# Kernel tuning notes

Hardware: AMD Instinct MI355X
Metric: run time of the kernel (lower is better)

The kernel has to match this reference:

```python
import jax, jax.numpy as jnp
import numpy as np

DN = ('NCHW', 'OIHW', 'NCHW')
EPS = 1e-5


def _conv(x, w, b, stride, pad):
    y = jax.lax.conv_general_dilated(x, w, (stride, stride), ((pad, pad), (pad, pad)), dimension_numbers=DN)
    return y + b[None, :, None, None]


def _convT(x, w, b):
    # PyTorch ConvTranspose2d(k=3, stride=2, padding=1, output_padding=1)
    # weight w: [in, out, kh, kw] -> flip spatial, swap in/out -> OIHW
    wt = jnp.flip(w, (2, 3)).transpose(1, 0, 2, 3)
    y = jax.lax.conv_general_dilated(x, wt, (1, 1), ((1, 2), (1, 2)), lhs_dilation=(2, 2), dimension_numbers=DN)
    return y + b[None, :, None, None]


def _inorm(x):
    # InstanceNorm2d, affine=False, biased variance (num_features arg unused since no affine)
    m = x.mean((2, 3), keepdims=True)
    v = ((x - m) ** 2).mean((2, 3), keepdims=True)
    return (x - m) / jnp.sqrt(v + EPS)


def _lrelu(x):
    return jnp.where(x >= 0, x, 0.2 * x)


def _refpad(x):
    return jnp.pad(x, ((0, 0), (0, 0), (1, 1), (1, 1)), mode='reflect')


def _backbone(image, w1, b1, w2, b2, w3, b3, wt, bt, w4, b4):
    x = _lrelu(_inorm(_conv(_refpad(image), w1, b1, 1, 0)))   # [B,32,H,W]
    x = _lrelu(_inorm(_conv(x, w2, b2, 2, 1)))                 # [B,64,H/2,W/2]
    x = _lrelu(_inorm(_conv(x, w3, b3, 2, 1)))                 # [B,128,H/4,W/4]
    x = _lrelu(_inorm(_convT(x, wt, bt)))                      # [B,256,H/2,W/2]
    x = jnp.tanh(_conv(_refpad(x), w4, b4, 1, 0))              # [B,512,H/2,W/2]
    return x


def _style_codes(x, seg):
    # nearest interpolation of seg to (h,w): src_idx = floor(dst * H / h)
    B, C, h, w = x.shape
    H, W = seg.shape[2], seg.shape[3]
    rows = (np.arange(h) * H) // h
    cols = (np.arange(w) * W) // w
    seg_ds = seg[:, :, rows][:, :, :, cols]                    # [B,L,h,w]
    m = (seg_ds != 0).astype(x.dtype)
    sums = jnp.einsum('bchw,blhw->blc', x, m)                  # segment sums
    counts = m.sum((2, 3))[..., None]                          # [B,L,1]
    return jnp.where(counts > 0, sums / jnp.maximum(counts, 1.0), 0.0)


def setup_inputs():
    key = jax.random.key(0)
    ks = jax.random.split(key, 8)
    B, H, W, L = 8, 256, 256, 19
    image = jax.random.normal(ks[0], (B, 3, H, W), jnp.float32)
    labels = jax.random.randint(ks[1], (B, H, W), 0, L)
    seg = jax.nn.one_hot(labels, L, axis=1, dtype=jnp.float32)  # one-hot semantic map
    def w(k, shape):
        return jax.random.normal(k, shape, jnp.float32) * 0.05
    return {
        'image': image, 'seg': seg,
        'w1': w(ks[2], (32, 3, 3, 3)), 'b1': jnp.zeros(32, jnp.float32),
        'w2': w(ks[3], (64, 32, 3, 3)), 'b2': jnp.zeros(64, jnp.float32),
        'w3': w(ks[4], (128, 64, 3, 3)), 'b3': jnp.zeros(128, jnp.float32),
        'wt': w(ks[5], (128, 256, 3, 3)), 'bt': jnp.zeros(256, jnp.float32),
        'w4': w(ks[6], (512, 256, 3, 3)), 'b4': jnp.zeros(512, jnp.float32),
    }


def reference(image, seg, w1, b1, w2, b2, w3, b3, wt, bt, w4, b4):
    x = _backbone(image, w1, b1, w2, b2, w3, b3, wt, bt, w4, b4)
    return _style_codes(x, seg)  # [B, label_nc, 512]
```

## Files before the change

### kernel.cpp

```cpp
#include <hip/hip_runtime.h>
#include <hip/hip_bf16.h>
#include <math.h>

typedef __attribute__((ext_vector_type(8))) short bf16x8;
typedef __attribute__((ext_vector_type(8))) unsigned short u16x8;
typedef __attribute__((ext_vector_type(4))) float f32x4;
typedef __attribute__((ext_vector_type(2))) long longx2;

#define OFF_X1   0ull
#define OFF_XQ8  0ull
#define OFF_X2   34080768ull
#define OFF_X3   51386368ull
#define OFF_Y4   60039168ull
#define OFF_WB8  127148032ull
#define OFF_WB2  129507328ull
#define OFF_WB3  129548288ull
#define OFF_WBT  129695744ull
#define OFF_ST1  130744320ull
#define OFF_ST2  130746368ull
#define OFF_ST3  130750464ull
#define OFF_ST4  130758656ull
#define OFF_SUMS 130775040ull
#define OFF_CNT  131086336ull
#define OFF_MS1  131086944ull
#define OFF_MS2  131088992ull
#define OFF_MS3  131093088ull
#define OFF_MS4  131101280ull
#define OFF_LAB  131117664ull
#define OFF_DWS  131641952ull
#define OFF_WSM  132166240ull
#define OFF_ST5  132690528ull
#define OFF_CB   132706912ull

__device__ __forceinline__ float bfu2f(unsigned short u) {
  return __builtin_bit_cast(float, ((unsigned)u) << 16);
}
__device__ __forceinline__ unsigned short f2bfu(float f) {
  __hip_bfloat16 h = __float2bfloat16(f);
  return __builtin_bit_cast(unsigned short, h);
}
__device__ __forceinline__ void gload_lds16(const void* g, void* l) {
  __builtin_amdgcn_global_load_lds(
      (const __attribute__((address_space(1))) unsigned int*)g,
      (__attribute__((address_space(3))) unsigned int*)l, 16, 0, 0);
}
template <bool HI>
__device__ __forceinline__ int cvtpk8(float a, float b, int old) {
  return __builtin_amdgcn_cvt_pk_fp8_f32(a, b, old, HI);
}
template <int SEL>
__device__ __forceinline__ float cvtf8(int v) {
  return __builtin_amdgcn_cvt_f32_fp8(v, SEL);
}

#define WAITV(N) asm volatile("s_waitcnt vmcnt(" #N ")" ::: "memory")

#define PIPE_STEP(WAITN, BUF, DOSTAGE, SNEXT)                 \
  asm volatile("s_waitcnt vmcnt(" #WAITN ")" ::: "memory");   \
  __builtin_amdgcn_s_barrier();                               \
  __builtin_amdgcn_sched_barrier(0);                          \
  mmaStep(BUF, (BUF) + 16384);                                \
  __builtin_amdgcn_sched_barrier(0);                          \
  __builtin_amdgcn_s_barrier();                               \
  if (DOSTAGE) stage(SNEXT, BUF);

__global__ __launch_bounds__(256) void conv1_k(const float* __restrict__ img,
                                               const float* __restrict__ w1,
                                               unsigned short* __restrict__ x1) {
  __shared__ float wl[864];
  int t = threadIdx.x, y = blockIdx.x, b = blockIdx.y;
  for (int i = t; i < 864; i += 256) wl[i] = w1[(i & 31) * 27 + (i >> 5)];
  __syncthreads();
  int x = t;
  float val[27];
  for (int ic = 0; ic < 3; ++ic) {
    const float* ip = img + ((size_t)(b * 3 + ic)) * 65536;
#pragma unroll
    for (int ky = 0; ky < 3; ++ky) {
      int gy = y - 1 + ky; gy = gy < 0 ? -gy : (gy > 255 ? 510 - gy : gy);
#pragma unroll
      for (int kx = 0; kx < 3; ++kx) {
        int gx = x - 1 + kx; gx = gx < 0 ? -gx : (gx > 255 ? 510 - gx : gx);
        val[ic * 9 + ky * 3 + kx] = ip[gy * 256 + gx];
      }
    }
  }
  float a[32];
#pragma unroll
  for (int oc = 0; oc < 32; ++oc) a[oc] = 0.f;
#pragma unroll
  for (int k = 0; k < 27; ++k) {
    float vv = val[k];
#pragma unroll
    for (int oc = 0; oc < 32; ++oc) a[oc] += wl[k * 32 + oc] * vv;
  }
  unsigned short ov[32];
#pragma unroll
  for (int oc = 0; oc < 32; ++oc) ov[oc] = f2bfu(a[oc]);
  unsigned short* op = x1 + ((size_t)(b * 258 + y + 1) * 258 + (x + 1)) * 32;
#pragma unroll
  for (int i = 0; i < 4; ++i) *(u16x8*)(op + i * 8) = *(const u16x8*)(ov + i * 8);
}

template <int C>
__global__ void statsn_k(const unsigned short* __restrict__ base, int rowStride, int unitsLog,
                         int rowsPer, long bStride, float* __restrict__ stats) {
  const int CH8 = C / 8;
  __shared__ float bins[C * 2];
  int tid = threadIdx.x, slice = blockIdx.x, b = blockIdx.y;
  for (int i = tid; i < C * 2; i += 256) bins[i] = 0.f;
  __syncthreads();
  const unsigned short* bp = base + (size_t)b * bStride + (size_t)(slice * rowsPer) * rowStride;
  int total = rowsPer << unitsLog;
  float s8[8] = {0, 0, 0, 0, 0, 0, 0, 0}, q8[8] = {0, 0, 0, 0, 0, 0, 0, 0};
  for (int idx = tid; idx < total; idx += 256) {
    int rl = idx >> unitsLog, ux = idx & ((1 << unitsLog) - 1);
    u16x8 v = *(const u16x8*)(bp + (size_t)rl * rowStride + ux * 8);
#pragma unroll
    for (int e = 0; e < 8; ++e) { float f = bfu2f(v[e]); s8[e] += f; q8[e] += f * f; }
  }
#pragma unroll
  for (int e = 0; e < 8; ++e)
    for (int off = 32; off >= CH8; off >>= 1) {
      s8[e] += __shfl_xor(s8[e], off);
      q8[e] += __shfl_xor(q8[e], off);
    }
  int lane = tid & 63;
  if (lane < CH8) {
#pragma unroll
    for (int e = 0; e < 8; ++e) {
      atomicAdd(&bins[(lane * 8 + e) * 2], s8[e]);
      atomicAdd(&bins[(lane * 8 + e) * 2 + 1], q8[e]);
    }
  }
  __syncthreads();
  for (int i = tid; i < C * 2; i += 256) atomicAdd(&stats[b * C * 2 + i], bins[i]);
}

__global__ void msn_k(const float* __restrict__ st, float2* __restrict__ ms, float invN, int total) {
  int i = blockIdx.x * 256 + threadIdx.x;
  if (i < total) {
    float m = st[2 * i] * invN;
    float v = st[2 * i + 1] * invN - m * m;
    ms[i] = make_float2(m, rsqrtf(fmaxf(v, 0.f) + 1e-5f));
  }
}

template <int C>
__global__ void nln_k(unsigned short* __restrict__ base, int rowStride, int unitsPerRow,
                      long bStride, const float2* __restrict__ ms) {
  const int CH8 = C / 8;
  int row = blockIdx.x, b = blockIdx.y;
  unsigned short* rp = base + (size_t)b * bStride + (size_t)row * rowStride;
  const float2* msb = ms + b * C;
  for (int idx = threadIdx.x; idx < unitsPerRow; idx += 256) {
    u16x8 v = *(u16x8*)(rp + idx * 8);
    int ch = (idx & (CH8 - 1)) * 8;
    u16x8 o;
#pragma unroll
    for (int e = 0; e < 8; ++e) {
      float2 m = msb[ch + e];
      float f = (bfu2f(v[e]) - m.x) * m.y;
      o[e] = f2bfu(f >= 0.f ? f : 0.2f * f);
    }
    *(u16x8*)(rp + idx * 8) = o;
  }
}

__global__ __launch_bounds__(256) void nln8_k(const unsigned short* __restrict__ y4,
                                              const float2* __restrict__ ms,
                                              unsigned char* __restrict__ xq8,
                                              float* __restrict__ st5) {
  __shared__ float bs[512];
  int t = threadIdx.x, row = blockIdx.x, b = blockIdx.y;
  int cg = t & 31, pg = t >> 5;
  int wof0 = (cg >> 4) * 128 + ((((cg & 15) & 3) << 2) | ((cg & 15) >> 2)) * 8;
  const float2* msb = ms + b * 256;
  float2 m0[8];
#pragma unroll
  for (int e = 0; e < 8; ++e) m0[e] = msb[cg * 8 + e];
  const unsigned short* rp = y4 + ((size_t)b * 16384 + row * 128) * 256;
  unsigned char* op = xq8 + ((size_t)b * 16384 + (size_t)row * 128) * 256;
  float s[8] = {0, 0, 0, 0, 0, 0, 0, 0}, d[8] = {0, 0, 0, 0, 0, 0, 0, 0};
  for (int i = 0; i < 16; ++i) {
    int px = pg * 16 + i;
    u16x8 v = *(const u16x8*)(rp + (size_t)px * 256 + cg * 8);
    float f[8];
#pragma unroll
    for (int e = 0; e < 8; ++e) {
      float x = (bfu2f(v[e]) - m0[e].x) * m0[e].y;
      f[e] = x >= 0.f ? x : 0.2f * x;
    }
    int lo = cvtpk8<false>(f[0], f[1], 0); lo = cvtpk8<true>(f[2], f[3], lo);
    int hi = cvtpk8<false>(f[4], f[5], 0); hi = cvtpk8<true>(f[6], f[7], hi);
    *(int*)(op + (size_t)px * 256 + wof0) = lo;
    *(int*)(op + (size_t)px * 256 + wof0 + 4) = hi;
    float fq;
    fq = cvtf8<0>(lo); s[0] += fq; d[0] += fq - f[0];
    fq = cvtf8<1>(lo); s[1] += fq; d[1] += fq - f[1];
    fq = cvtf8<2>(lo); s[2] += fq; d[2] += fq - f[2];
    fq = cvtf8<3>(lo); s[3] += fq; d[3] += fq - f[3];
    fq = cvtf8<0>(hi); s[4] += fq; d[4] += fq - f[4];
    fq = cvtf8<1>(hi); s[5] += fq; d[5] += fq - f[5];
    fq = cvtf8<2>(hi); s[6] += fq; d[6] += fq - f[6];
    fq = cvtf8<3>(hi); s[7] += fq; d[7] += fq - f[7];
  }
  for (int i = t; i < 512; i += 256) bs[i] = 0.f;
  __syncthreads();
#pragma unroll
  for (int e = 0; e < 8; ++e) {
    atomicAdd(&bs[cg * 8 + e], s[e]);
    atomicAdd(&bs[256 + cg * 8 + e], d[e]);
  }
  __syncthreads();
  for (int i = t; i < 512; i += 256) atomicAdd(&st5[b * 512 + i], bs[i]);
}

__global__ void wrep2_k(const float* __restrict__ w2, unsigned short* __restrict__ wb2) {
  int idx = blockIdx.x * 256 + threadIdx.x;
  if (idx >= 20480) return;
  int oc = idx / 320, r = idx % 320, tap = r >> 5, ic = r & 31;
  wb2[idx] = tap < 9 ? f2bfu(w2[(oc * 32 + ic) * 9 + tap]) : (unsigned short)0;
}
__global__ void wrep3_k(const float* __restrict__ w3, unsigned short* __restrict__ wb3) {
  int idx = blockIdx.x * 256 + threadIdx.x;
  int oc = idx / 576, r = idx % 576, tap = r >> 6, ic = r & 63;
  wb3[idx] = f2bfu(w3[(oc * 64 + ic) * 9 + tap]);
}
__device__ const int c_taptab[16] = {4, -1, -1, -1, 5, 3, -1, -1, 7, -1, 1, -1, 8, 6, 2, 0};
__global__ void wrepT_k(const float* __restrict__ wt, unsigned short* __restrict__ wbt) {
  int idx = blockIdx.x * 256 + threadIdx.x;
  int n = idx >> 9, k = idx & 511;
  int cl = n >> 8, oc = n & 255, nb = k >> 7, ic = k & 127;
  int tap = c_taptab[cl * 4 + nb];
  wbt[idx] = tap < 0 ? (unsigned short)0 : f2bfu(wt[(ic * 256 + oc) * 9 + tap]);
}
__global__ __launch_bounds__(256) void dwrep_k(const float* __restrict__ w4,
                                               unsigned char* __restrict__ wb8,
                                               float* __restrict__ dws,
                                               float* __restrict__ wsum) {
  int oc = blockIdx.x, ic = threadIdx.x;
  int local = ic & 127;
  int p = (ic & 128) + ((local >> 3) & 3) * 32 + ((local >> 5) & 3) * 8 + (local & 7);
  float ds = 0.f, ws = 0.f;
  for (int kk = 0; kk < 9; ++kk) {
    float w = w4[(size_t)oc * 2304 + ic * 9 + kk];
    int pk = cvtpk8<false>(w, 0.f, 0);
    wb8[((size_t)oc * 9 + kk) * 256 + p] = (unsigned char)(pk & 0xff);
    float wq = cvtf8<0>(pk);
    ds += wq - w; ws += w;
  }
  dws[oc * 256 + ic] = ds;
  wsum[oc * 256 + ic] = ws;
}

__global__ __launch_bounds__(256) void cbias_k(const float* __restrict__ st5,
                                               const float* __restrict__ dws,
                                               const float* __restrict__ wsum,
                                               float* __restrict__ cb) {
  int oc = blockIdx.x, b = blockIdx.y, t = threadIdx.x;
  const float inv = 1.f / 16384.f;
  float muq = st5[b * 512 + t] * inv;
  float dmu = st5[b * 512 + 256 + t] * inv;
  float a = muq * dws[oc * 256 + t] + dmu * wsum[oc * 256 + t];
#pragma unroll
  for (int o = 1; o < 64; o <<= 1) a += __shfl_xor(a, o);
  __shared__ float r[4];
  if ((t & 63) == 0) r[t >> 6] = a;
  __syncthreads();
  if (t == 0) cb[b * 512 + oc] = r[0] + r[1] + r[2] + r[3];
}

__global__ __launch_bounds__(256) void conv2_k(const unsigned short* __restrict__ x1,
                                               const unsigned short* __restrict__ wb2,
                                               unsigned short* __restrict__ x2,
                                               float* __restrict__ st2) {
  __shared__ char smem[49664];
  float* bins = (float*)(smem + 49152);
  int tid = threadIdx.x, y = blockIdx.x, b = blockIdx.y;
  int lane = tid & 63, w = tid >> 6, wm = w >> 1, wn = w & 1;
  int lr = lane & 15, lg = lane >> 4;
  f32x4 acc[4][2];
#pragma unroll
  for (int i = 0; i < 4; ++i)
#pragma unroll
    for (int j = 0; j < 2; ++j) acc[i][j] = (f32x4){0.f, 0.f, 0.f, 0.f};

  int rowA[4], lcA[4], PbA[4];
#pragma unroll
  for (int i = 0; i < 4; ++i) {
    int pb = i * 256 + tid;
    PbA[i] = pb * 16; rowA[i] = pb >> 3; lcA[i] = (pb & 7) ^ (rowA[i] & 7);
  }
  int rowB[2], lcB[2], PbB[2];
#pragma unroll
  for (int i = 0; i < 2; ++i) {
    int pb = i * 256 + tid;
    PbB[i] = pb * 16; rowB[i] = pb >> 3; lcB[i] = (pb & 7) ^ (rowB[i] & 7);
  }
  const unsigned short* xb = x1 + (size_t)b * 2130048;

  auto stage = [&](int kb, char* base) {
    char* As = base;
    char* Bs = base + 16384;
#pragma unroll
    for (int i = 0; i < 4; ++i) {
      int tp = kb * 2 + (lcA[i] >> 2);
      int ky = (tp * 11) >> 5;
      int kx = tp - ky * 3;
      gload_lds16(xb + ((size_t)((2 * y + ky) * 258 + 2 * rowA[i] + kx)) * 32 + (lcA[i] & 3) * 8,
                  As + PbA[i]);
    }
#pragma unroll
    for (int i = 0; i < 2; ++i)
      gload_lds16(wb2 + rowB[i] * 320 + kb * 64 + lcB[i] * 8, Bs + PbB[i]);
  };

  stage(0, smem);
  __syncthreads();
  for (int kb = 0; kb < 5; ++kb) {
    char* base = smem + (kb & 1) * 24576;
    if (kb + 1 < 5) stage(kb + 1, smem + ((kb + 1) & 1) * 24576);
    char* As = base;
    char* Bs = base + 16384;
    bf16x8 af[4][2], bfr[2][2];
#pragma unroll
    for (int mi = 0; mi < 4; ++mi)
#pragma unroll
      for (int kh = 0; kh < 2; ++kh) {
        int row = wm * 64 + mi * 16 + lr;
        int byte = row * 128 + ((kh * 64 + lg * 16) ^ ((row & 7) << 4));
        af[mi][kh] = *(const bf16x8*)(As + byte);
      }
#pragma unroll
    for (int ni = 0; ni < 2; ++ni)
#pragma unroll
      for (int kh = 0; kh < 2; ++kh) {
        int row = wn * 32 + ni * 16 + lr;
        int byte = row * 128 + ((kh * 64 + lg * 16) ^ ((row & 7) << 4));
        bfr[ni][kh] = *(const bf16x8*)(Bs + byte);
      }
#pragma unroll
    for (int mi = 0; mi < 4; ++mi)
#pragma unroll
      for (int ni = 0; ni < 2; ++ni)
#pragma unroll
        for (int kh = 0; kh < 2; ++kh)
          acc[mi][ni] = __builtin_amdgcn_mfma_f32_16x16x32_bf16(af[mi][kh], bfr[ni][kh],
                                                                acc[mi][ni], 0, 0, 0);
    __syncthreads();
  }

  if (tid < 128) bins[tid] = 0.f;
  __syncthreads();
  unsigned short* ob = x2 + (size_t)b * 1081600;
#pragma unroll
  for (int ni = 0; ni < 2; ++ni) {
    int oc = wn * 32 + ni * 16 + lr;
    float s = 0.f, q = 0.f;
#pragma unroll
    for (int mi = 0; mi < 4; ++mi)
#pragma unroll
      for (int r = 0; r < 4; ++r) {
        int m = wm * 64 + mi * 16 + lg * 4 + r;
        float v = acc[mi][ni][r];
        ob[((y + 1) * 130 + m + 1) * 64 + oc] = f2bfu(v);
        s += v; q += v * v;
      }
    atomicAdd(&bins[oc * 2], s);
    atomicAdd(&bins[oc * 2 + 1], q);
  }
  __syncthreads();
  if (tid < 128) atomicAdd(&st2[b * 128 + tid], bins[tid]);
}

__global__ __launch_bounds__(256) void conv3_k(const unsigned short* __restrict__ x2,
                                               const unsigned short* __restrict__ wb3,
                                               unsigned short* __restrict__ x3,
                                               float* __restrict__ st3) {
  __shared__ char smem[66560];
  float* bins = (float*)(smem + 65536);
  int tid = threadIdx.x, y0 = blockIdx.x * 2, b = blockIdx.y;
  int lane = tid & 63, w = tid >> 6, wm = w >> 1, wn = w & 1;
  int lr = lane & 15, lg = lane >> 4;
  f32x4 acc[4][4];
#pragma unroll
  for (int i = 0; i < 4; ++i)
#pragma unroll
    for (int j = 0; j < 4; ++j) acc[i][j] = (f32x4){0.f, 0.f, 0.f, 0.f};

  int rowS[4], lc[4], Pb[4];
#pragma unroll
  for (int i = 0; i < 4; ++i) {
    int pb = i * 256 + tid;
    Pb[i] = pb * 16; rowS[i] = pb >> 3; lc[i] = (pb & 7) ^ (rowS[i] & 7);
  }
  const unsigned short* xb = x2 + (size_t)b * 1081600;

  auto stage = [&](int kk, char* base) {
    int ky = kk / 3, kx = kk - ky * 3;
#pragma unroll
    for (int i = 0; i < 4; ++i) {
      int m = rowS[i], di = m >> 6, xx = m & 63;
      gload_lds16(xb + ((size_t)((2 * (y0 + di) + ky) * 130 + 2 * xx + kx)) * 64 + lc[i] * 8,
                  base + Pb[i]);
    }
#pragma unroll
    for (int i = 0; i < 4; ++i)
      gload_lds16(wb3 + (rowS[i] * 9 + kk) * 64 + lc[i] * 8, base + 16384 + Pb[i]);
  };

  stage(0, smem);
  __syncthreads();
  for (int kk = 0; kk < 9; ++kk) {
    char* base = smem + (kk & 1) * 32768;
    if (kk + 1 < 9) stage(kk + 1, smem + ((kk + 1) & 1) * 32768);
    char* As = base;
    char* Bs = base + 16384;
    bf16x8 af[4][2], bfr[4][2];
#pragma unroll
    for (int mi = 0; mi < 4; ++mi)
#pragma unroll
      for (int kh = 0; kh < 2; ++kh) {
        int row = wm * 64 + mi * 16 + lr;
        int byte = row * 128 + ((kh * 64 + lg * 16) ^ ((row & 7) << 4));
        af[mi][kh] = *(const bf16x8*)(As + byte);
      }
#pragma unroll
    for (int ni = 0; ni < 4; ++ni)
#pragma unroll
      for (int kh = 0; kh < 2; ++kh) {
        int row = wn * 64 + ni * 16 + lr;
        int byte = row * 128 + ((kh * 64 + lg * 16) ^ ((row & 7) << 4));
        bfr[ni][kh] = *(const bf16x8*)(Bs + byte);
      }
#pragma unroll
    for (int mi = 0; mi < 4; ++mi)
#pragma unroll
      for (int ni = 0; ni < 4; ++ni)
#pragma unroll
        for (int kh = 0; kh < 2; ++kh)
          acc[mi][ni] = __builtin_amdgcn_mfma_f32_16x16x32_bf16(af[mi][kh], bfr[ni][kh],
                                                                acc[mi][ni], 0, 0, 0);
    __syncthreads();
  }

  if (tid < 256) bins[tid] = 0.f;
  __syncthreads();
  unsigned short* ob = x3 + (size_t)b * 540800;
#pragma unroll
  for (int ni = 0; ni < 4; ++ni) {
    int oc = wn * 64 + ni * 16 + lr;
    float s = 0.f, q = 0.f;
#pragma unroll
    for (int mi = 0; mi < 4; ++mi)
#pragma unroll
      for (int r = 0; r < 4; ++r) {
        int m = wm * 64 + mi * 16 + lg * 4 + r;
        int di = m >> 6, xx = m & 63;
        float v = acc[mi][ni][r];
        ob[((y0 + di) * 65 + xx) * 128 + oc] = f2bfu(v);
        s += v; q += v * v;
      }
    atomicAdd(&bins[oc * 2], s);
    atomicAdd(&bins[oc * 2 + 1], q);
  }
  __syncthreads();
  if (tid < 256) atomicAdd(&st3[b * 256 + tid], bins[tid]);
}

__global__ __launch_bounds__(256) void convT_k(const unsigned short* __restrict__ x3,
                                               const unsigned short* __restrict__ wbt,
                                               unsigned short* __restrict__ y4,
                                               float* __restrict__ st4) {
  __shared__ char smem[67584];
  float* bins = (float*)(smem + 65536);
  int tid = threadIdx.x, i0 = blockIdx.x * 2, nblk = blockIdx.y, b = blockIdx.z;
  int n0 = nblk * 128, cl = nblk >> 1, och0 = (nblk & 1) * 128;
  int lane = tid & 63, w = tid >> 6, wm = w >> 1, wn = w & 1;
  int lr = lane & 15, lg = lane >> 4;
  f32x4 acc[4][4];
#pragma unroll
  for (int i = 0; i < 4; ++i)
#pragma unroll
    for (int j = 0; j < 4; ++j) acc[i][j] = (f32x4){0.f, 0.f, 0.f, 0.f};

  int rowS[4], lc[4], Pb[4];
#pragma unroll
  for (int i = 0; i < 4; ++i) {
    int pb = i * 256 + tid;
    Pb[i] = pb * 16; rowS[i] = pb >> 3; lc[i] = (pb & 7) ^ (rowS[i] & 7);
  }
  int aoff[4][2], boff[4][2];
#pragma unroll
  for (int mi = 0; mi < 4; ++mi)
#pragma unroll
    for (int kh = 0; kh < 2; ++kh) {
      int row = wm * 64 + mi * 16 + lr;
      aoff[mi][kh] = row * 128 + ((kh * 64 + lg * 16) ^ ((row & 7) << 4));
      int rowb = wn * 64 + mi * 16 + lr;
      boff[mi][kh] = rowb * 128 + ((kh * 64 + lg * 16) ^ ((rowb & 7) << 4));
    }
  const unsigned short* xb = x3 + (size_t)b * 540800;

  auto stage = [&](int kb, char* base) {
    int nb = kb >> 1, chalf = (kb & 1) * 64;
#pragma unroll
    for (int i = 0; i < 4; ++i) {
      int m = rowS[i], di = m >> 6, j = m & 63;
      int pi = i0 + di + (nb >> 1), pj = j + (nb & 1);
      gload_lds16(xb + ((size_t)(pi * 65 + pj)) * 128 + chalf + lc[i] * 8, base + Pb[i]);
    }
#pragma unroll
    for (int i = 0; i < 4; ++i)
      gload_lds16(wbt + (size_t)(n0 + rowS[i]) * 512 + kb * 64 + lc[i] * 8,
                  base + 16384 + Pb[i]);
  };

  auto mmaStep = [&](char* As, char* Bs) {
    bf16x8 af[4][2], bfr[4][2];
#pragma unroll
    for (int mi = 0; mi < 4; ++mi)
#pragma unroll
      for (int kh = 0; kh < 2; ++kh) af[mi][kh] = *(const bf16x8*)(As + aoff[mi][kh]);
#pragma unroll
    for (int ni = 0; ni < 4; ++ni)
#pragma unroll
      for (int kh = 0; kh < 2; ++kh) bfr[ni][kh] = *(const bf16x8*)(Bs + boff[ni][kh]);
#pragma unroll
    for (int mi = 0; mi < 4; ++mi)
#pragma unroll
      for (int ni = 0; ni < 4; ++ni)
#pragma unroll
        for (int kh = 0; kh < 2; ++kh)
          acc[mi][ni] = __builtin_amdgcn_mfma_f32_16x16x32_bf16(af[mi][kh], bfr[ni][kh],
                                                                acc[mi][ni], 0, 0, 0);
  };

  char* B0 = smem;
  char* B1 = smem + 32768;
  stage(0, B0);
  stage(1, B1);
  for (int sp = 0; sp < 3; ++sp) {
    PIPE_STEP(8, B0, true, 2 * sp + 2);
    PIPE_STEP(8, B1, true, 2 * sp + 3);
  }
  PIPE_STEP(8, B0, false, 0);
  PIPE_STEP(0, B1, false, 0);

  if (tid < 256) bins[tid] = 0.f;
  __syncthreads();
  unsigned short* ob = y4 + (size_t)b * 4194304;
  int dy = cl >> 1, dx = cl & 1;
#pragma unroll
  for (int ni = 0; ni < 4; ++ni) {
    int loc = wn * 64 + ni * 16 + lr;
    int oc = och0 + loc;
    float s = 0.f, q = 0.f;
#pragma unroll
    for (int mi = 0; mi < 4; ++mi)
#pragma unroll
      for (int r = 0; r < 4; ++r) {
        int m = wm * 64 + mi * 16 + lg * 4 + r;
        int di = m >> 6, j = m & 63;
        int oy = 2 * (i0 + di) + dy, ox = 2 * j + dx;
        float v = acc[mi][ni][r];
        ob[(oy * 128 + ox) * 256 + oc] = f2bfu(v);
        s += v; q += v * v;
      }
    atomicAdd(&bins[loc * 2], s);
    atomicAdd(&bins[loc * 2 + 1], q);
  }
  __syncthreads();
  if (tid < 256) atomicAdd(&st4[b * 512 + och0 * 2 + tid], bins[tid]);
}

__global__ void lab_k(const float* __restrict__ seg, int* __restrict__ lab,
                      float* __restrict__ counts) {
  __shared__ int hist[19];
  int t = threadIdx.x;
  if (t < 19) hist[t] = 0;
  __syncthreads();
  int b = blockIdx.y;
  int p = blockIdx.x * 256 + t;
  int i = p >> 7, j = p & 127;
  const float* sp = seg + (size_t)b * 19 * 65536 + (2 * i) * 256 + 2 * j;
  int l = 0;
  for (int k = 0; k < 19; ++k) { if (sp[(size_t)k * 65536] != 0.f) { l = k; break; } }
  lab[b * 16384 + p] = l;
  atomicAdd(&hist[l], 1);
  __syncthreads();
  if (t < 19) atomicAdd(&counts[b * 19 + t], (float)hist[t]);
}

__global__ __launch_bounds__(256, 3) void conv4_k(
    const unsigned char* __restrict__ xq8, const unsigned char* __restrict__ wb8,
    const float* __restrict__ b4, const float* __restrict__ cb,
    const int* __restrict__ lab, float* __restrict__ sums) {
  __shared__ char smem[33280];
  char* As = smem;
  char* Bs = smem + 16384;
  int* labs = (int*)(smem + 32768);
  int tid = threadIdx.x;
  int id = blockIdx.x;
  int b = id & 7, rr = id >> 3;
  int y = rr >> 2, nblk = rr & 3;
  int n0 = nblk * 128;
  if (tid < 128) labs[tid] = lab[b * 16384 + y * 128 + tid];
  int lane = tid & 63, w = tid >> 6;
  int wm = w >> 1, wn = w & 1;
  int lr = lane & 15, lg = lane >> 4;

  f32x4 acc[4][4];
#pragma unroll
  for (int i = 0; i < 4; ++i)
#pragma unroll
    for (int j = 0; j < 4; ++j) acc[i][j] = (f32x4){0.f, 0.f, 0.f, 0.f};

  const unsigned char* xb = xq8 + (size_t)b * 4194304;

  int rs0 = tid >> 3;
  int csw = ((tid & 7) ^ (rs0 & 7)) << 4;
  int ldoff = tid * 16;

  const unsigned char* brow[4];
#pragma unroll
  for (int i = 0; i < 4; ++i)
    brow[i] = wb8 + (size_t)(n0 + rs0 + 32 * i) * 2304 + csw;

  int koff = 0;
  for (int kk = 0; kk < 9; ++kk) {
    int ky = (kk * 11) >> 5, kx = kk - ky * 3;
    int sy = y + ky - 1; sy = sy < 0 ? 1 : (sy > 127 ? 126 : sy);
    const unsigned char* arow[4];
#pragma unroll
    for (int i = 0; i < 4; ++i) {
      int sx = rs0 + 32 * i + kx - 1;
      sx = sx < 0 ? 1 : (sx > 127 ? 126 : sx);
      arow[i] = xb + ((size_t)(sy * 128 + sx)) * 256 + csw;
    }
    for (int ic0 = 0; ic0 < 256; ic0 += 128) {
      __syncthreads();
#pragma unroll
      for (int i = 0; i < 4; ++i) gload_lds16(arow[i] + ic0, As + i * 4096 + ldoff);
#pragma unroll
      for (int i = 0; i < 4; ++i) gload_lds16(brow[i] + koff, Bs + i * 4096 + ldoff);
      koff += 128;
      __syncthreads();

      longx2 bq[4][2];
#pragma unroll
      for (int ni = 0; ni < 4; ++ni) {
        int row = wn * 64 + ni * 16 + lr;
#pragma unroll
        for (int k2 = 0; k2 < 2; ++k2) {
          int byte = row * 128 + ((lg * 32 + k2 * 16) ^ ((row & 7) << 4));
          bq[ni][k2] = *(const longx2*)(Bs + byte);
        }
      }
#pragma unroll
      for (int mi = 0; mi < 4; ++mi) {
        int row = wm * 64 + mi * 16 + lr;
        longx2 aq[2];
#pragma unroll
        for (int k2 = 0; k2 < 2; ++k2) {
          int byte = row * 128 + ((lg * 32 + k2 * 16) ^ ((row & 7) << 4));
          aq[k2] = *(const longx2*)(As + byte);
        }
#pragma unroll
        for (int ni = 0; ni < 4; ++ni)
#pragma unroll
          for (int k2 = 0; k2 < 2; ++k2) {
            acc[mi][ni] = __builtin_amdgcn_mfma_f32_16x16x32_fp8_fp8(
                aq[k2][0], bq[ni][k2][0], acc[mi][ni], 0, 0, 0);
            acc[mi][ni] = __builtin_amdgcn_mfma_f32_16x16x32_fp8_fp8(
                aq[k2][1], bq[ni][k2][1], acc[mi][ni], 0, 0, 0);
          }
      }
    }
  }

  __syncthreads();
  float* bins = (float*)smem;
  for (int t2 = tid; t2 < 19 * 128; t2 += 256) bins[t2] = 0.f;
  __syncthreads();
  float bias[4];
#pragma unroll
  for (int ni = 0; ni < 4; ++ni) {
    int gc = n0 + wn * 64 + ni * 16 + lr;
    bias[ni] = b4[gc] - cb[b * 512 + gc];
  }
#pragma unroll
  for (int mi = 0; mi < 4; ++mi)
#pragma unroll
    for (int ni = 0; ni < 4; ++ni) {
      int ct = wn * 64 + ni * 16 + lr;
#pragma unroll
      for (int r = 0; r < 4; ++r) {
        int x = wm * 64 + mi * 16 + lg * 4 + r;
        float v = tanhf(acc[mi][ni][r] + bias[ni]);
        atomicAdd(&bins[labs[x] * 128 + ct], v);
      }
    }
  __syncthreads();
  for (int t2 = tid; t2 < 19 * 128; t2 += 256) {
    float v = bins[t2];
    if (v != 0.f)
      atomicAdd(&sums[((size_t)(b * 19 + (t2 >> 7))) * 512 + n0 + (t2 & 127)], v);
  }
}

__global__ void finalize_k(const float* __restrict__ sums, const float* __restrict__ counts,
                           float* __restrict__ out) {
  int idx = blockIdx.x * 256 + threadIdx.x;
  int bl = idx / 512;
  float c = counts[bl];
  out[idx] = c > 0.f ? sums[idx] / fmaxf(c, 1.f) : 0.f;
}

extern "C" void kernel_launch(void* const* d_in, const int* in_sizes, int n_in,
                              void* d_out, int out_size, void* d_ws, size_t ws_size,
                              hipStream_t stream) {
  const float* image = (const float*)d_in[0];
  const float* seg   = (const float*)d_in[1];
  const float* w1    = (const float*)d_in[2];
  const float* w2    = (const float*)d_in[4];
  const float* w3    = (const float*)d_in[6];
  const float* wt    = (const float*)d_in[8];
  const float* w4    = (const float*)d_in[10];
  const float* b4    = (const float*)d_in[11];
  float* out = (float*)d_out;
  char* ws = (char*)d_ws;

  unsigned short* x1  = (unsigned short*)(ws + OFF_X1);
  unsigned char*  xq8 = (unsigned char*)(ws + OFF_XQ8);
  unsigned short* x2  = (unsigned short*)(ws + OFF_X2);
  unsigned short* x3  = (unsigned short*)(ws + OFF_X3);
  unsigned short* y4  = (unsigned short*)(ws + OFF_Y4);
  unsigned char*  wb8 = (unsigned char*)(ws + OFF_WB8);
  unsigned short* wb2 = (unsigned short*)(ws + OFF_WB2);
  unsigned short* wb3 = (unsigned short*)(ws + OFF_WB3);
  unsigned short* wbt = (unsigned short*)(ws + OFF_WBT);
  float* st1 = (float*)(ws + OFF_ST1);
  float* st2 = (float*)(ws + OFF_ST2);
  float* st3 = (float*)(ws + OFF_ST3);
  float* st4 = (float*)(ws + OFF_ST4);
  float* sums = (float*)(ws + OFF_SUMS);
  float* counts = (float*)(ws + OFF_CNT);
  float2* ms1 = (float2*)(ws + OFF_MS1);
  float2* ms2 = (float2*)(ws + OFF_MS2);
  float2* ms3 = (float2*)(ws + OFF_MS3);
  float2* ms4 = (float2*)(ws + OFF_MS4);
  int* lab = (int*)(ws + OFF_LAB);
  float* dws  = (float*)(ws + OFF_DWS);
  float* wsum = (float*)(ws + OFF_WSM);
  float* st5  = (float*)(ws + OFF_ST5);
  float* cbv  = (float*)(ws + OFF_CB);

  hipMemsetAsync(ws, 0, 60039168, stream);
  hipMemsetAsync(ws + OFF_ST1, 0, 342624, stream);
  hipMemsetAsync(ws + OFF_ST5, 0, 16384, stream);

  wrep2_k<<<80, 256, 0, stream>>>(w2, wb2);
  wrep3_k<<<288, 256, 0, stream>>>(w3, wb3);
  wrepT_k<<<2048, 256, 0, stream>>>(wt, wbt);
  dwrep_k<<<512, 256, 0, stream>>>(w4, wb8, dws, wsum);
  lab_k<<<dim3(64, 8), 256, 0, stream>>>(seg, lab, counts);

  conv1_k<<<dim3(256, 8), 256, 0, stream>>>(image, w1, x1);
  statsn_k<32><<<dim3(16, 8), 256, 0, stream>>>(x1 + 259 * 32, 258 * 32, 10, 16, 2130048L, st1);
  msn_k<<<1, 256, 0, stream>>>(st1, ms1, 1.f / 65536.f, 256);
  nln_k<32><<<dim3(256, 8), 256, 0, stream>>>(x1 + 259 * 32, 258 * 32, 1024, 2130048L, ms1);

  conv2_k<<<dim3(128, 8), 256, 0, stream>>>(x1, wb2, x2, st2);
  msn_k<<<2, 256, 0, stream>>>(st2, ms2, 1.f / 16384.f, 512);
  nln_k<64><<<dim3(128, 8), 256, 0, stream>>>(x2 + 131 * 64, 130 * 64, 1024, 1081600L, ms2);

  conv3_k<<<dim3(32, 8), 256, 0, stream>>>(x2, wb3, x3, st3);
  msn_k<<<4, 256, 0, stream>>>(st3, ms3, 1.f / 4096.f, 1024);
  nln_k<128><<<dim3(64, 8), 256, 0, stream>>>(x3, 65 * 128, 1024, 540800L, ms3);

  convT_k<<<dim3(32, 8, 8), 256, 0, stream>>>(x3, wbt, y4, st4);
  msn_k<<<8, 256, 0, stream>>>(st4, ms4, 1.f / 16384.f, 2048);

  nln8_k<<<dim3(128, 8), 256, 0, stream>>>(y4, ms4, xq8, st5);
  cbias_k<<<dim3(512, 8), 256, 0, stream>>>(st5, dws, wsum, cbv);

  conv4_k<<<4096, 256, 0, stream>>>(xq8, wb8, b4, cbv, lab, sums);

  finalize_k<<<304, 256, 0, stream>>>(sums, counts, out);
}
```

Baseline: 770.0 us.

## Restructure conv4 into 256x256 tiles with double-buffered async LDS pipeline

The fp8 implicit-GEMM conv4 kernel moves from 128x128 tiles with 256 threads and synchronous staging to 256x256 tiles with 512 threads. Global-to-LDS loads now go through a double-buffered 128KB pipeline that prefetches the next K slice in quarters, interleaved with MFMA phases. It also sets s_setprio around the MFMA blocks. Larger tiles raise data reuse and the pipelining hides load latency, at the cost of lower occupancy (one block per CU due to LDS) and higher register pressure from 32 accumulators.

```diff
diff --git a/kernel.cpp b/kernel.cpp
--- a/kernel.cpp
+++ b/kernel.cpp
@@ -54,6 +54,7 @@
 }
 
 #define WAITV(N) asm volatile("s_waitcnt vmcnt(" #N ")" ::: "memory")
+#define WAITL0   asm volatile("s_waitcnt lgkmcnt(0)" ::: "memory")
 
 #define PIPE_STEP(WAITN, BUF, DOSTAGE, SNEXT)                 \
   asm volatile("s_waitcnt vmcnt(" #WAITN ")" ::: "memory");   \
@@ -593,96 +594,167 @@
   if (t < 19) atomicAdd(&counts[b * 19 + t], (float)hist[t]);
 }
 
-__global__ __launch_bounds__(256, 3) void conv4_k(
+#define TILE4F(CUR, NXT, TN, DOSTAGE, W1, W2, W3)                                   \
+  {                                                                                 \
+    longx2 af[4][2], bq0[2][2], bq1[2][2];                                          \
+                                                              \
+    WAITV(W1);                                                                      \
+    __builtin_amdgcn_s_barrier();                                                   \
+    __builtin_amdgcn_sched_barrier(0);                                              \
+    _Pragma("unroll") for (int i = 0; i < 4; ++i)                                   \
+      _Pragma("unroll") for (int k = 0; k < 2; ++k)                                 \
+        af[i][k] = *(const longx2*)((CUR) + aoff[i][k]);                            \
+    _Pragma("unroll") for (int j = 0; j < 2; ++j)                                   \
+      _Pragma("unroll") for (int k = 0; k < 2; ++k)                                 \
+        bq0[j][k] = *(const longx2*)((CUR) + boff[j][k]);                           \
+    if (DOSTAGE) stageA2(TN, NXT, 0);                                               \
+    WAITL0;                                                                         \
+    __builtin_amdgcn_sched_barrier(0);                                              \
+    __builtin_amdgcn_s_setprio(1);                                                  \
+    _Pragma("unroll") for (int i = 0; i < 4; ++i)                                   \
+      _Pragma("unroll") for (int j = 0; j < 2; ++j)                                 \
+        _Pragma("unroll") for (int k = 0; k < 2; ++k) {                             \
+          acc[i][j] = __builtin_amdgcn_mfma_f32_16x16x32_fp8_fp8(                   \
+              af[i][k][0], bq0[j][k][0], acc[i][j], 0, 0, 0);                       \
+          acc[i][j] = __builtin_amdgcn_mfma_f32_16x16x32_fp8_fp8(                   \
+              af[i][k][1], bq0[j][k][1], acc[i][j], 0, 0, 0);                       \
+        }                                                                           \
+    __builtin_amdgcn_s_setprio(0);                                                  \
+                                                              \
+    WAITV(W2);                                                                      \
+    __builtin_amdgcn_s_barrier();                                                   \
+    __builtin_amdgcn_sched_barrier(0);                                              \
+    _Pragma("unroll") for (int j = 0; j < 2; ++j)                                   \
+      _Pragma("unroll") for (int k = 0; k < 2; ++k)                                 \
+        bq1[j][k] = *(const longx2*)((CUR) + boff[2 + j][k]);                       \
+    if (DOSTAGE) stageB2(TN, NXT, 0);                                               \
+    WAITL0;                                                                         \
+    __builtin_amdgcn_sched_barrier(0);                                              \
+    __builtin_amdgcn_s_setprio(1);                                                  \
+    _Pragma("unroll") for (int i = 0; i < 4; ++i)                                   \
+      _Pragma("unroll") for (int j = 0; j < 2; ++j)                                 \
+        _Pragma("unroll") for (int k = 0; k < 2; ++k) {                             \
+          acc[i][2 + j] = __builtin_amdgcn_mfma_f32_16x16x32_fp8_fp8(               \
+              af[i][k][0], bq1[j][k][0], acc[i][2 + j], 0, 0, 0);                   \
+          acc[i][2 + j] = __builtin_amdgcn_mfma_f32_16x16x32_fp8_fp8(               \
+              af[i][k][1], bq1[j][k][1], acc[i][2 + j], 0, 0, 0);                   \
+        }                                                                           \
+    __builtin_amdgcn_s_setprio(0);                                                  \
+                                                              \
+    WAITV(W3);                                                                      \
+    __builtin_amdgcn_s_barrier();                                                   \
+    __builtin_amdgcn_sched_barrier(0);                                              \
+    _Pragma("unroll") for (int i = 0; i < 4; ++i)                                   \
+      _Pragma("unroll") for (int k = 0; k < 2; ++k)                                 \
+        af[i][k] = *(const longx2*)((CUR) + aoff[4 + i][k]);                        \
+    if (DOSTAGE) stageB2(TN, NXT, 1);                                               \
+    WAITL0;                                                                         \
+    __builtin_amdgcn_sched_barrier(0);                                              \
+    __builtin_amdgcn_s_setprio(1);                                                  \
+    _Pragma("unroll") for (int i = 0; i < 4; ++i)                                   \
+      _Pragma("unroll") for (int j = 0; j < 2; ++j)                                 \
+        _Pragma("unroll") for (int k = 0; k < 2; ++k) {                             \
+          acc[4 + i][j] = __builtin_amdgcn_mfma_f32_16x16x32_fp8_fp8(               \
+              af[i][k][0], bq0[j][k][0], acc[4 + i][j], 0, 0, 0);                   \
+          acc[4 + i][j] = __builtin_amdgcn_mfma_f32_16x16x32_fp8_fp8(               \
+              af[i][k][1], bq0[j][k][1], acc[4 + i][j], 0, 0, 0);                   \
+        }                                                                           \
+    __builtin_amdgcn_s_setprio(0);                                                  \
+                                \
+    if (DOSTAGE) stageA2(TN, NXT, 1);                                               \
+    __builtin_amdgcn_s_setprio(1);                                                  \
+    _Pragma("unroll") for (int i = 0; i < 4; ++i)                                   \
+      _Pragma("unroll") for (int j = 0; j < 2; ++j)                                 \
+        _Pragma("unroll") for (int k = 0; k < 2; ++k) {                             \
+          acc[4 + i][2 + j] = __builtin_amdgcn_mfma_f32_16x16x32_fp8_fp8(           \
+              af[i][k][0], bq1[j][k][0], acc[4 + i][2 + j], 0, 0, 0);               \
+          acc[4 + i][2 + j] = __builtin_amdgcn_mfma_f32_16x16x32_fp8_fp8(           \
+              af[i][k][1], bq1[j][k][1], acc[4 + i][2 + j], 0, 0, 0);               \
+        }                                                                           \
+    __builtin_amdgcn_s_setprio(0);                                                  \
+  }
+
+__global__ __launch_bounds__(512) void conv4_k(
     const unsigned char* __restrict__ xq8, const unsigned char* __restrict__ wb8,
     const float* __restrict__ b4, const float* __restrict__ cb,
     const int* __restrict__ lab, float* __restrict__ sums) {
-  __shared__ char smem[33280];
-  char* As = smem;
-  char* Bs = smem + 16384;
-  int* labs = (int*)(smem + 32768);
+  __shared__ char smem[132096];
+  int* labs = (int*)(smem + 131072);
   int tid = threadIdx.x;
   int id = blockIdx.x;
   int b = id & 7, rr = id >> 3;
-  int y = rr >> 2, nblk = rr & 3;
-  int n0 = nblk * 128;
-  if (tid < 128) labs[tid] = lab[b * 16384 + y * 128 + tid];
+  int nblk = rr & 1, y0 = (rr >> 1) * 2;
+  int n0 = nblk * 256;
+  if (tid < 256) labs[tid] = lab[b * 16384 + (y0 + (tid >> 7)) * 128 + (tid & 127)];
   int lane = tid & 63, w = tid >> 6;
-  int wm = w >> 1, wn = w & 1;
+  int wm = w >> 2, wn = w & 3;
   int lr = lane & 15, lg = lane >> 4;
 
-  f32x4 acc[4][4];
-#pragma unroll
-  for (int i = 0; i < 4; ++i)
+  f32x4 acc[8][4];
+#pragma unroll
+  for (int i = 0; i < 8; ++i)
 #pragma unroll
     for (int j = 0; j < 4; ++j) acc[i][j] = (f32x4){0.f, 0.f, 0.f, 0.f};
 
   const unsigned char* xb = xq8 + (size_t)b * 4194304;
 
-  int rs0 = tid >> 3;
-  int csw = ((tid & 7) ^ (rs0 & 7)) << 4;
-  int ldoff = tid * 16;
-
-  const unsigned char* brow[4];
-#pragma unroll
-  for (int i = 0; i < 4; ++i)
-    brow[i] = wb8 + (size_t)(n0 + rs0 + 32 * i) * 2304 + csw;
-
-  int koff = 0;
-  for (int kk = 0; kk < 9; ++kk) {
+  auto stageA2 = [&](int t, char* tb, int h) {
+    int kk = t >> 1, ic0 = (t & 1) << 7;
     int ky = (kk * 11) >> 5, kx = kk - ky * 3;
-    int sy = y + ky - 1; sy = sy < 0 ? 1 : (sy > 127 ? 126 : sy);
-    const unsigned char* arow[4];
-#pragma unroll
-    for (int i = 0; i < 4; ++i) {
-      int sx = rs0 + 32 * i + kx - 1;
-      sx = sx < 0 ? 1 : (sx > 127 ? 126 : sx);
-      arow[i] = xb + ((size_t)(sy * 128 + sx)) * 256 + csw;
-    }
-    for (int ic0 = 0; ic0 < 256; ic0 += 128) {
-      __syncthreads();
-#pragma unroll
-      for (int i = 0; i < 4; ++i) gload_lds16(arow[i] + ic0, As + i * 4096 + ldoff);
-#pragma unroll
-      for (int i = 0; i < 4; ++i) gload_lds16(brow[i] + koff, Bs + i * 4096 + ldoff);
-      koff += 128;
-      __syncthreads();
-
-      longx2 bq[4][2];
-#pragma unroll
-      for (int ni = 0; ni < 4; ++ni) {
-        int row = wn * 64 + ni * 16 + lr;
-#pragma unroll
-        for (int k2 = 0; k2 < 2; ++k2) {
-          int byte = row * 128 + ((lg * 32 + k2 * 16) ^ ((row & 7) << 4));
-          bq[ni][k2] = *(const longx2*)(Bs + byte);
-        }
-      }
-#pragma unroll
-      for (int mi = 0; mi < 4; ++mi) {
-        int row = wm * 64 + mi * 16 + lr;
-        longx2 aq[2];
-#pragma unroll
-        for (int k2 = 0; k2 < 2; ++k2) {
-          int byte = row * 128 + ((lg * 32 + k2 * 16) ^ ((row & 7) << 4));
-          aq[k2] = *(const longx2*)(As + byte);
-        }
-#pragma unroll
-        for (int ni = 0; ni < 4; ++ni)
-#pragma unroll
-          for (int k2 = 0; k2 < 2; ++k2) {
-            acc[mi][ni] = __builtin_amdgcn_mfma_f32_16x16x32_fp8_fp8(
-                aq[k2][0], bq[ni][k2][0], acc[mi][ni], 0, 0, 0);
-            acc[mi][ni] = __builtin_amdgcn_mfma_f32_16x16x32_fp8_fp8(
-                aq[k2][1], bq[ni][k2][1], acc[mi][ni], 0, 0, 0);
-          }
-      }
-    }
-  }
+#pragma unroll
+    for (int l = 0; l < 2; ++l) {
+      int u = l * 1024 + h * 512 + tid;
+      int m = u >> 3, c = (u & 7) ^ (m & 7);
+      int sy = y0 + (m >> 7) + ky - 1; sy = sy < 0 ? 1 : (sy > 127 ? 126 : sy);
+      int sx = (m & 127) + kx - 1; sx = sx < 0 ? 1 : (sx > 127 ? 126 : sx);
+      gload_lds16(xb + (size_t)(sy * 128 + sx) * 256 + ic0 + c * 16, tb + u * 16);
+    }
+  };
+  auto stageB2 = [&](int t, char* tb, int q) {
+    int kk = t >> 1, ic0 = (t & 1) << 7;
+#pragma unroll
+    for (int l = 0; l < 2; ++l) {
+      int u = l * 1024 + ((tid & 256) << 1) + (q << 8) + (tid & 255);
+      int n = u >> 3, c = (u & 7) ^ (n & 7);
+      gload_lds16(wb8 + (size_t)(n0 + n) * 2304 + kk * 256 + ic0 + c * 16,
+                  tb + 32768 + u * 16);
+    }
+  };
+
+  int aoff[8][2], boff[4][2];
+#pragma unroll
+  for (int mi = 0; mi < 8; ++mi)
+#pragma unroll
+    for (int k2 = 0; k2 < 2; ++k2) {
+      int row = wm * 128 + mi * 16 + lr;
+      aoff[mi][k2] = row * 128 + ((lg * 32 + k2 * 16) ^ ((row & 7) << 4));
+    }
+#pragma unroll
+  for (int ni = 0; ni < 4; ++ni)
+#pragma unroll
+    for (int k2 = 0; k2 < 2; ++k2) {
+      int row = wn * 64 + ni * 16 + lr;
+      boff[ni][k2] = 32768 + row * 128 + ((lg * 32 + k2 * 16) ^ ((row & 7) << 4));
+    }
+
+  char* buf0 = smem;
+  char* buf1 = smem + 65536;
+
+  stageA2(0, buf0, 0);
+  stageB2(0, buf0, 0);
+  stageB2(0, buf0, 1);
+  stageA2(0, buf0, 1);
+
+  for (int tt = 0; tt < 8; ++tt) {
+    TILE4F(buf0, buf1, 2 * tt + 1, true, 4, 4, 4);
+    TILE4F(buf1, buf0, 2 * tt + 2, true, 4, 4, 4);
+  }
+  TILE4F(buf0, buf1, 17, true, 4, 4, 4);
+  TILE4F(buf1, buf0, 0, false, 4, 2, 0);
 
   __syncthreads();
   float* bins = (float*)smem;
-  for (int t2 = tid; t2 < 19 * 128; t2 += 256) bins[t2] = 0.f;
+  for (int i = tid; i < 19 * 256; i += 512) bins[i] = 0.f;
   __syncthreads();
   float bias[4];
 #pragma unroll
@@ -691,22 +763,22 @@
     bias[ni] = b4[gc] - cb[b * 512 + gc];
   }
 #pragma unroll
-  for (int mi = 0; mi < 4; ++mi)
+  for (int mi = 0; mi < 8; ++mi)
 #pragma unroll
     for (int ni = 0; ni < 4; ++ni) {
       int ct = wn * 64 + ni * 16 + lr;
 #pragma unroll
       for (int r = 0; r < 4; ++r) {
-        int x = wm * 64 + mi * 16 + lg * 4 + r;
+        int m = wm * 128 + mi * 16 + lg * 4 + r;
         float v = tanhf(acc[mi][ni][r] + bias[ni]);
-        atomicAdd(&bins[labs[x] * 128 + ct], v);
+        atomicAdd(&bins[labs[m] * 256 + ct], v);
       }
     }
   __syncthreads();
-  for (int t2 = tid; t2 < 19 * 128; t2 += 256) {
-    float v = bins[t2];
+  for (int i = tid; i < 19 * 256; i += 512) {
+    float v = bins[i];
     if (v != 0.f)
-      atomicAdd(&sums[((size_t)(b * 19 + (t2 >> 7))) * 512 + n0 + (t2 & 127)], v);
+      atomicAdd(&sums[((size_t)(b * 19 + (i >> 8))) * 512 + n0 + (i & 255)], v);
   }
 }
 
@@ -786,7 +858,7 @@
   nln8_k<<<dim3(128, 8), 256, 0, stream>>>(y4, ms4, xq8, st5);
   cbias_k<<<dim3(512, 8), 256, 0, stream>>>(st5, dws, wsum, cbv);
 
-  conv4_k<<<4096, 256, 0, stream>>>(xq8, wb8, b4, cbv, lab, sums);
+  conv4_k<<<1024, 512, 0, stream>>>(xq8, wb8, b4, cbv, lab, sums);
 
   finalize_k<<<304, 256, 0, stream>>>(sums, counts, out);
 }
```

Result: slower. 918.9 us (+19.3%).
